# Optimization experiments

Measured on AMD Instinct MI355X. Metric: run time of the kernel, lower is better.

## Reference

```python
import jax, jax.numpy as jnp
import numpy as np

LSTM_IN = 125
LSTM_H = 125
MLP_D_H = 512
N = 512


def _lstm_scan(x, Wih, Whh, bih, bhh):
    # x: (N, LSTM_IN); PyTorch gate order: i, f, g, o
    H = LSTM_H
    def step(carry, xt):
        h, c = carry
        g = Wih @ xt + Whh @ h + bih + bhh  # (4H,)
        i = jax.nn.sigmoid(g[:H])
        f = jax.nn.sigmoid(g[H:2 * H])
        gg = jnp.tanh(g[2 * H:3 * H])
        o = jax.nn.sigmoid(g[3 * H:])
        c = f * c + i * gg
        h = o * jnp.tanh(c)
        return (h, c), h
    init = (jnp.zeros((H,), x.dtype), jnp.zeros((H,), x.dtype))
    _, hs = jax.lax.scan(step, init, x)
    return hs  # (N, H)


def setup_inputs() -> dict:
    key = jax.random.key(0)
    ks = jax.random.split(key, 14)
    s = 0.05
    d = {
        "sentence_emb": jax.random.normal(ks[0], (N, 1, LSTM_IN), jnp.float32),
        "Wih_f": jax.random.normal(ks[1], (4 * LSTM_H, LSTM_IN), jnp.float32) * s,
        "Whh_f": jax.random.normal(ks[2], (4 * LSTM_H, LSTM_H), jnp.float32) * s,
        "bih_f": jax.random.normal(ks[3], (4 * LSTM_H,), jnp.float32) * s,
        "bhh_f": jax.random.normal(ks[4], (4 * LSTM_H,), jnp.float32) * s,
        "Wih_b": jax.random.normal(ks[5], (4 * LSTM_H, LSTM_IN), jnp.float32) * s,
        "Whh_b": jax.random.normal(ks[6], (4 * LSTM_H, LSTM_H), jnp.float32) * s,
        "bih_b": jax.random.normal(ks[7], (4 * LSTM_H,), jnp.float32) * s,
        "bhh_b": jax.random.normal(ks[8], (4 * LSTM_H,), jnp.float32) * s,
        "W1": jax.random.normal(ks[9], (MLP_D_H, 4 * LSTM_H), jnp.float32) * s,
        "b1": jax.random.normal(ks[10], (MLP_D_H,), jnp.float32) * s,
        "W2": jax.random.normal(ks[11], (1, MLP_D_H), jnp.float32) * s,
        "b2": jax.random.normal(ks[12], (1,), jnp.float32) * s,
    }
    return d


def reference(sentence_emb, Wih_f, Whh_f, bih_f, bhh_f, Wih_b, Whh_b, bih_b, bhh_b, W1, b1, W2, b2):
    x = sentence_emb[:, 0, :]  # (N, 125), batch=1
    h_fwd = _lstm_scan(x, Wih_f, Whh_f, bih_f, bhh_f)           # (N, 125)
    h_bwd = _lstm_scan(x[::-1], Wih_b, Whh_b, bih_b, bhh_b)[::-1]  # (N, 125)
    h = jnp.concatenate([h_fwd, h_bwd], axis=-1)  # (N, 250)
    # output_mtx[i, j] = MLP(concat(h[j], h[i]))
    # Decompose first linear: W1 @ cat(h_j, h_i) = Wa @ h_j + Wb @ h_i
    D = h.shape[-1]
    Pa = h @ W1[:, :D].T   # (N, H): contribution of h_j
    Pb = h @ W1[:, D:].T   # (N, H): contribution of h_i
    hidden = jnp.tanh(Pb[:, None, :] + Pa[None, :, :] + b1)  # (N, N, H)
    out = hidden @ W2[0] + b2[0]  # (N, N)
    return out
```

## Files before the change

### kernel.cpp

```cpp
#include <hip/hip_runtime.h>

typedef __bf16 bf16_t;
typedef __bf16 bf16x8 __attribute__((ext_vector_type(8)));
typedef float f32x4 __attribute__((ext_vector_type(4)));
typedef int   int4v __attribute__((ext_vector_type(4)));

#define LOG2E 1.4426950408889634f

template<int CTRL>
__device__ __forceinline__ float qperm(float x) {
  return __builtin_bit_cast(float,
      __builtin_amdgcn_update_dpp(0, __builtin_bit_cast(int, x), CTRL, 0xF, 0xF, true));
}

__device__ __forceinline__ void lds_barrier() {
  asm volatile("s_waitcnt lgkmcnt(0)\n\ts_barrier" ::: "memory");
}

__global__ __launch_bounds__(256) void pre_kernel(
    const float* __restrict__ x,
    const float* __restrict__ Wih_f, const float* __restrict__ bih_f,
    const float* __restrict__ bhh_f,
    const float* __restrict__ Wih_b, const float* __restrict__ bih_b,
    const float* __restrict__ bhh_b,
    float* __restrict__ preT)
{
  const int dir = blockIdx.x >> 5;
  const int T   = blockIdx.x & 31;
  const float* __restrict__ Wih = dir ? Wih_b : Wih_f;
  const float* __restrict__ bih = dir ? bih_b : bih_f;
  const float* __restrict__ bhh = dir ? bhh_b : bhh_f;

  const int tid = threadIdx.x;
  const int wv  = tid >> 6;
  const int lane = tid & 63;
  const int q = lane >> 4, cc = lane & 15;

  const int r  = 16 * T + cc;
  const int na = r >> 2, pa = r & 3;
  const bool vld = (na < 125);
  const float* __restrict__ Wr = Wih + (vld ? (125 * pa + na) * 125 : 0);

  bf16x8 whi[4], wlo[4];
  #pragma unroll
  for (int ks = 0; ks < 4; ++ks) {
    #pragma unroll
    for (int j = 0; j < 8; ++j) {
      int k = 32 * ks + 8 * q + j;
      float wvv = (vld && k < 125) ? Wr[k] : 0.0f;
      bf16_t hi = (bf16_t)wvv;
      whi[ks][j] = hi;
      wlo[ks][j] = (bf16_t)(wvv - (float)hi);
    }
  }

  float bias[4];
  #pragma unroll
  for (int reg = 0; reg < 4; ++reg) {
    int ro = 16 * T + 4 * q + reg;
    int no = ro >> 2, po = ro & 3;
    bias[reg] = (no < 125) ? (bih[125 * po + no] + bhh[125 * po + no]) : 0.0f;
  }

  for (int i = 0; i < 8; ++i) {
    const int tt = 8 * wv + i;
    const int t  = 16 * tt + cc;
    const int trow = dir ? (511 - t) : t;
    const float* __restrict__ xr = x + trow * 125;

    f32x4 acc = (f32x4)0.0f;
    #pragma unroll
    for (int ks = 0; ks < 4; ++ks) {
      bf16x8 xhi, xlo;
      #pragma unroll
      for (int j = 0; j < 8; ++j) {
        int k = 32 * ks + 8 * q + j;
        float xv = (k < 125) ? xr[k] : 0.0f;
        bf16_t hi = (bf16_t)xv;
        xhi[j] = hi;
        xlo[j] = (bf16_t)(xv - (float)hi);
      }
      acc = __builtin_amdgcn_mfma_f32_16x16x32_bf16(whi[ks], xhi, acc, 0, 0, 0);
      acc = __builtin_amdgcn_mfma_f32_16x16x32_bf16(whi[ks], xlo, acc, 0, 0, 0);
      acc = __builtin_amdgcn_mfma_f32_16x16x32_bf16(wlo[ks], xhi, acc, 0, 0, 0);
    }
    #pragma unroll
    for (int reg = 0; reg < 4; ++reg) {
      int ro = 16 * T + 4 * q + reg;
      preT[dir * 262144 + ro * 512 + 16 * tt + cc] = acc[reg] + bias[reg];
    }
  }
}

__global__ __launch_bounds__(512) void lstm_kernel(
    const float* __restrict__ Whh_f, const float* __restrict__ Whh_b,
    const float* __restrict__ pre,
    bf16_t* __restrict__ h_all)
{
  const int dir = blockIdx.x;
  const float* __restrict__ Whh = dir ? Whh_b : Whh_f;

  const int tid  = threadIdx.x;
  const int lane = tid & 63;
  const int w    = tid >> 6;
  const int q    = lane >> 4;
  const int cc   = lane & 15;
  const int lt   = cc >> 2;
  const int p    = cc & 3;

  float wm = 0.0f;
  #pragma unroll
  for (int LT = 0; LT < 4; ++LT) {
    int rr = 16 * (4 * w + LT) + cc;
    int nn = rr >> 2, pp = rr & 3;
    if (nn < 125) {
      const float* __restrict__ Wrow = Whh + (125 * pp + nn) * 125;
      #pragma unroll
      for (int ks = 0; ks < 2; ++ks)
        #pragma unroll
        for (int jj = 0; jj < 16; ++jj) {
          int k = 64 * ks + 16 * q + jj;
          if (k < 125) wm = fmaxf(wm, fabsf(Wrow[k]));
        }
    }
  }
  #pragma unroll
  for (int off = 1; off < 64; off <<= 1)
    wm = fmaxf(wm, __shfl_xor(wm, off));
  __shared__ float wmx[8];
  if (lane == 0) wmx[w] = wm;
  __syncthreads();
  float wmax = wmx[0];
  #pragma unroll
  for (int u = 1; u < 8; ++u) wmax = fmaxf(wmax, wmx[u]);
  const float s_w  = 127.0f / wmax;
  const float invq = wmax / (127.0f * 127.0f);

  int4v afrag[4][2];
  #pragma unroll
  for (int LT = 0; LT < 4; ++LT) {
    int rr = 16 * (4 * w + LT) + cc;
    int nn = rr >> 2, pp = rr & 3;
    bool avld = (nn < 125);
    const float* __restrict__ Wrow = Whh + (avld ? (125 * pp + nn) * 125 : 0);
    #pragma unroll
    for (int ks = 0; ks < 2; ++ks) {
      int4v v;
      #pragma unroll
      for (int word = 0; word < 4; ++word) {
        int b = 0;
        #pragma unroll
        for (int byte = 0; byte < 4; ++byte) {
          int jj = 4 * word + byte;
          int k  = 64 * ks + 16 * q + jj;
          int qv = 0;
          if (avld && k < 125)
            qv = (int)__builtin_rintf(Wrow[k] * s_w);
          b |= (qv & 0xFF) << (8 * byte);
        }
        v[word] = b;
      }
      afrag[LT][ks] = v;
    }
  }

  __shared__ __align__(16) char hbuf[2][128];
  if (tid < 256) hbuf[tid >> 7][tid & 127] = 0;
  if (dir == 0) {
    #pragma unroll
    for (int u = 0; u < 6; ++u) h_all[tid * 256 + 250 + u] = (bf16_t)0.0f;
  }
  __syncthreads();

  const int   r_lane = 64 * w + 16 * lt + 4 * q + p;
  const int   nset   = 16 * w + 4 * lt + q;
  const float mult   = (p == 2) ? (-2.0f * LOG2E) : (-LOG2E);
  const float sA     = (p == 2) ? 2.0f : 1.0f;
  const float sB     = (p == 2) ? -1.0f : 0.0f;
  const float dscale = mult * invq;
  const float* __restrict__ preR = pre + dir * 262144 + r_lane * 512;
  float c = 0.0f;

  float4 pv_cur = *(const float4*)preR;

  for (int g = 0; g < 128; ++g) {
    float4 pv_nxt = make_float4(0.f, 0.f, 0.f, 0.f);
    if (g < 127) pv_nxt = *(const float4*)(preR + 4 * (g + 1));

    #pragma unroll
    for (int s4 = 0; s4 < 4; ++s4) {
      const int step = 4 * g + s4;
      const int cur  = s4 & 1, nxt = cur ^ 1;
      const float pv = (s4 == 0) ? pv_cur.x : (s4 == 1) ? pv_cur.y
                     : (s4 == 2) ? pv_cur.z : pv_cur.w;
      const float pvm = mult * pv;

      int4v b0 = *(const int4v*)&hbuf[cur][16 * q];
      int4v b1 = *(const int4v*)&hbuf[cur][64 + 16 * q];

      int4v acc[4];
      #pragma unroll
      for (int LT = 0; LT < 4; ++LT) {
        int4v a = (int4v)0;
        a = __builtin_amdgcn_mfma_i32_16x16x64_i8(afrag[LT][0], b0, a, 0, 0, 0);
        a = __builtin_amdgcn_mfma_i32_16x16x64_i8(afrag[LT][1], b1, a, 0, 0, 0);
        acc[LT] = a;
      }

      int gl[4];
      #pragma unroll
      for (int LT = 0; LT < 4; ++LT) {
        int a01 = (p & 1) ? acc[LT][1] : acc[LT][0];
        int a23 = (p & 1) ? acc[LT][3] : acc[LT][2];
        gl[LT] = (p & 2) ? a23 : a01;
      }
      int b01 = (lt & 1) ? gl[1] : gl[0];
      int b23 = (lt & 1) ? gl[3] : gl[2];
      int gsel = (lt & 2) ? b23 : b01;

      float gf  = (float)gsel;
      float xg  = fmaf(gf, dscale, pvm);
      float e   = __builtin_amdgcn_exp2f(xg);
      float y   = __builtin_amdgcn_rcpf(1.0f + e);
      float act = fmaf(y, sA, sB);

      float b_i = qperm<0x00>(act);
      float b_f = qperm<0x55>(act);
      float b_g = qperm<0xAA>(act);
      float b_o = qperm<0xFF>(act);
      c = fmaf(b_f, c, b_i * b_g);
      float e2 = __builtin_amdgcn_exp2f(-2.0f * LOG2E * c);
      float tc = fmaf(__builtin_amdgcn_rcpf(1.0f + e2), 2.0f, -1.0f);
      float h  = b_o * tc;

      if (p == 0) {
        int qh = (int)__builtin_rintf(h * 127.0f);
        hbuf[nxt][nset] = (char)qh;
        if (nset < 125) {
          int t_orig = dir ? (511 - step) : step;
          h_all[t_orig * 256 + dir * 125 + nset] = (bf16_t)h;
        }
      }
      lds_barrier();
    }
    pv_cur = pv_nxt;
  }
}

__global__ __launch_bounds__(256) void qgemm_kernel(
    const bf16_t* __restrict__ h_all,
    const float* __restrict__ W1,
    const float* __restrict__ b1,
    float* __restrict__ Ea,
    float* __restrict__ Eb)
{
  const int tid  = threadIdx.x;
  const int wv   = tid >> 6;
  const int lane = tid & 63;
  const int q    = lane >> 4, cc = lane & 15;
  const int bj   = blockIdx.x & 31;
  const int bm   = blockIdx.x >> 5;
  const int m    = bm * 64 + wv * 16 + cc;
  const int j0   = bj * 16;
  const int jA   = j0 + cc;

  const bool isB = (m >= 512);
  const int  row = isB ? (m - 512) : m;
  const int  cof = isB ? 250 : 0;

  f32x4 acc = (f32x4)0.0f;
  #pragma unroll
  for (int ks = 0; ks < 8; ++ks) {
    int kb = 32 * ks + 8 * q;
    bf16x8 a = *(const bf16x8*)&h_all[jA * 256 + kb];
    bf16x8 b;
    #pragma unroll
    for (int jj = 0; jj < 8; ++jj) {
      int k = kb + jj;
      float v = (k < 250) ? W1[row * 500 + cof + k] : 0.0f;
      b[jj] = (bf16_t)v;
    }
    acc = __builtin_amdgcn_mfma_f32_16x16x32_bf16(a, b, acc, 0, 0, 0);
  }

  const float C2 = 2.0f * LOG2E;
  #pragma unroll
  for (int reg = 0; reg < 4; ++reg) {
    int j = j0 + 4 * q + reg;
    float v = acc[reg];
    if (!isB) Ea[j * 512 + m] = __builtin_amdgcn_exp2f(C2 * v);
    else      Eb[j * 512 + (m - 512)] =
                  __builtin_amdgcn_exp2f(C2 * (v + b1[m - 512]));
  }
}

__global__ __launch_bounds__(256) void outer_kernel(
    const float* __restrict__ Ea, const float* __restrict__ Eb,
    const float* __restrict__ W2, const float* __restrict__ b2,
    float* __restrict__ out)
{
  __shared__ float sa[2][32][33];
  __shared__ float sb[2][32][33];
  __shared__ float sw[2][32];

  const int tid = threadIdx.x;
  const int bi  = blockIdx.x >> 4, bjx = blockIdx.x & 15;
  const int i0  = bi * 32, j0 = bjx * 32;
  const int ii0 = (tid & 15) * 2;
  const int jj0 = (tid >> 4) * 2;
  const int ljj = tid & 31, kk4 = (tid >> 5) * 4;

  float accR[2][2] = {{0.0f, 0.0f}, {0.0f, 0.0f}};
  float wsum = 0.0f;

  for (int kc = 0; kc < 16; ++kc) {
    const int buf = kc & 1;
    const int k0  = kc * 32;
    float4 va = *(const float4*)&Ea[(j0 + ljj) * 512 + k0 + kk4];
    float4 vb = *(const float4*)&Eb[(i0 + ljj) * 512 + k0 + kk4];
    sa[buf][kk4 + 0][ljj] = va.x; sa[buf][kk4 + 1][ljj] = va.y;
    sa[buf][kk4 + 2][ljj] = va.z; sa[buf][kk4 + 3][ljj] = va.w;
    sb[buf][kk4 + 0][ljj] = vb.x; sb[buf][kk4 + 1][ljj] = vb.y;
    sb[buf][kk4 + 2][ljj] = vb.z; sb[buf][kk4 + 3][ljj] = vb.w;
    if (tid < 32) sw[buf][tid] = W2[k0 + tid];
    __syncthreads();

    #pragma unroll 4
    for (int kk = 0; kk < 32; ++kk) {
      float2 av = *(const float2*)&sa[buf][kk][jj0];
      float2 bv = *(const float2*)&sb[buf][kk][ii0];
      float wk = sw[buf][kk];
      wsum += wk;
      {
        float e = av.x * bv.x;
        accR[0][0] = fmaf(wk, __builtin_amdgcn_rcpf(1.0f + e), accR[0][0]);
      }
      {
        float e = av.y * bv.x;
        accR[0][1] = fmaf(wk, __builtin_amdgcn_rcpf(1.0f + e), accR[0][1]);
      }
      {
        float e = av.x * bv.y;
        accR[1][0] = fmaf(wk, __builtin_amdgcn_rcpf(1.0f + e), accR[1][0]);
      }
      {
        float e = av.y * bv.y;
        accR[1][1] = fmaf(wk, __builtin_amdgcn_rcpf(1.0f + e), accR[1][1]);
      }
    }
  }

  const float bb = b2[0];
  #pragma unroll
  for (int i2 = 0; i2 < 2; ++i2)
    #pragma unroll
    for (int j2 = 0; j2 < 2; ++j2)
      out[(i0 + ii0 + i2) * 512 + (j0 + jj0 + j2)] =
          wsum - 2.0f * accR[i2][j2] + bb;
}

extern "C" void kernel_launch(void* const* d_in, const int* in_sizes, int n_in,
                              void* d_out, int out_size, void* d_ws, size_t ws_size,
                              hipStream_t stream) {
  const float* emb   = (const float*)d_in[0];
  const float* Wih_f = (const float*)d_in[1];
  const float* Whh_f = (const float*)d_in[2];
  const float* bih_f = (const float*)d_in[3];
  const float* bhh_f = (const float*)d_in[4];
  const float* Wih_b = (const float*)d_in[5];
  const float* Whh_b = (const float*)d_in[6];
  const float* bih_b = (const float*)d_in[7];
  const float* bhh_b = (const float*)d_in[8];
  const float* W1    = (const float*)d_in[9];
  const float* b1    = (const float*)d_in[10];
  const float* W2    = (const float*)d_in[11];
  const float* b2    = (const float*)d_in[12];
  float* out = (float*)d_out;

  char* ws = (char*)d_ws;
  float*  pre   = (float*)ws;
  bf16_t* h_all = (bf16_t*)(ws + 2 * 1024 * 1024);
  float*  Ea    = (float*)(ws + 2 * 1024 * 1024 + 256 * 1024);
  float*  Eb    = Ea + 512 * 512;

  pre_kernel<<<64, 256, 0, stream>>>(emb, Wih_f, bih_f, bhh_f,
                                     Wih_b, bih_b, bhh_b, pre);
  lstm_kernel<<<2, 512, 0, stream>>>(Whh_f, Whh_b, pre, h_all);
  qgemm_kernel<<<512, 256, 0, stream>>>(h_all, W1, b1, Ea, Eb);
  outer_kernel<<<256, 256, 0, stream>>>(Ea, Eb, W2, b2, out);
}
```

Baseline: 324.8 us.

## Pair k-terms in outer kernel to halve reciprocals and retile to 16x32 blocks

The outer tanh-MLP kernel now folds two consecutive k terms into one fraction, (w1*t2 + w2*t1)/(t1*t2), so each pair of hidden units needs one rcp instead of two. Tiles shrink to 16x32 outputs per block, with each thread computing two outputs, and the grid doubles to 512 blocks. Shared memory is switched to row-major k-contiguous storage so global loads can be written with float4 stores. The trade-off is a risk of overflow in the product of two exponentials when values are large, and smaller tiles that reuse each loaded value less.

```diff
diff --git a/kernel.cpp b/kernel.cpp
--- a/kernel.cpp
+++ b/kernel.cpp
@@ -299,64 +299,64 @@
     const float* __restrict__ W2, const float* __restrict__ b2,
     float* __restrict__ out)
 {
-  __shared__ float sa[2][32][33];
-  __shared__ float sb[2][32][33];
+  __shared__ float sa2[2][32][36];
+  __shared__ float sb2[2][16][36];
   __shared__ float sw[2][32];
 
   const int tid = threadIdx.x;
-  const int bi  = blockIdx.x >> 4, bjx = blockIdx.x & 15;
-  const int i0  = bi * 32, j0 = bjx * 32;
-  const int ii0 = (tid & 15) * 2;
-  const int jj0 = (tid >> 4) * 2;
-  const int ljj = tid & 31, kk4 = (tid >> 5) * 4;
-
-  float accR[2][2] = {{0.0f, 0.0f}, {0.0f, 0.0f}};
+  const int bi  = blockIdx.x >> 4;
+  const int bjx = blockIdx.x & 15;
+  const int i0  = bi * 16, j0 = bjx * 32;
+  const int ii  = tid & 15;
+  const int jj2 = tid >> 4;
+
+  const int lj  = tid & 31, lk4 = (tid >> 5) * 4;
+  const int li  = tid & 15, lk4b = ((tid >> 4) & 7) * 4;
+
+  float accR0 = 0.0f, accR1 = 0.0f;
   float wsum = 0.0f;
 
   for (int kc = 0; kc < 16; ++kc) {
     const int buf = kc & 1;
     const int k0  = kc * 32;
-    float4 va = *(const float4*)&Ea[(j0 + ljj) * 512 + k0 + kk4];
-    float4 vb = *(const float4*)&Eb[(i0 + ljj) * 512 + k0 + kk4];
-    sa[buf][kk4 + 0][ljj] = va.x; sa[buf][kk4 + 1][ljj] = va.y;
-    sa[buf][kk4 + 2][ljj] = va.z; sa[buf][kk4 + 3][ljj] = va.w;
-    sb[buf][kk4 + 0][ljj] = vb.x; sb[buf][kk4 + 1][ljj] = vb.y;
-    sb[buf][kk4 + 2][ljj] = vb.z; sb[buf][kk4 + 3][ljj] = vb.w;
+    float4 va = *(const float4*)&Ea[(j0 + lj) * 512 + k0 + lk4];
+    *(float4*)&sa2[buf][lj][lk4] = va;
+    if (tid < 128) {
+      float4 vb = *(const float4*)&Eb[(i0 + li) * 512 + k0 + lk4b];
+      *(float4*)&sb2[buf][li][lk4b] = vb;
+    }
     if (tid < 32) sw[buf][tid] = W2[k0 + tid];
     __syncthreads();
 
     #pragma unroll 4
-    for (int kk = 0; kk < 32; ++kk) {
-      float2 av = *(const float2*)&sa[buf][kk][jj0];
-      float2 bv = *(const float2*)&sb[buf][kk][ii0];
-      float wk = sw[buf][kk];
-      wsum += wk;
+    for (int kk = 0; kk < 32; kk += 2) {
+      float2 wv = *(const float2*)&sw[buf][kk];
+      float2 bv = *(const float2*)&sb2[buf][ii][kk];
+      float2 a0 = *(const float2*)&sa2[buf][2 * jj2 + 0][kk];
+      float2 a1 = *(const float2*)&sa2[buf][2 * jj2 + 1][kk];
+      wsum += wv.x + wv.y;
       {
-        float e = av.x * bv.x;
-        accR[0][0] = fmaf(wk, __builtin_amdgcn_rcpf(1.0f + e), accR[0][0]);
+        float t1  = fmaf(a0.x, bv.x, 1.0f);
+        float t2  = fmaf(a0.y, bv.y, 1.0f);
+        float den = t1 * t2;
+        float num = fmaf(wv.x, t2, wv.y * t1);
+        accR0 = fmaf(num, __builtin_amdgcn_rcpf(den), accR0);
       }
       {
-        float e = av.y * bv.x;
-        accR[0][1] = fmaf(wk, __builtin_amdgcn_rcpf(1.0f + e), accR[0][1]);
-      }
-      {
-        float e = av.x * bv.y;
-        accR[1][0] = fmaf(wk, __builtin_amdgcn_rcpf(1.0f + e), accR[1][0]);
-      }
-      {
-        float e = av.y * bv.y;
-        accR[1][1] = fmaf(wk, __builtin_amdgcn_rcpf(1.0f + e), accR[1][1]);
+        float t1  = fmaf(a1.x, bv.x, 1.0f);
+        float t2  = fmaf(a1.y, bv.y, 1.0f);
+        float den = t1 * t2;
+        float num = fmaf(wv.x, t2, wv.y * t1);
+        accR1 = fmaf(num, __builtin_amdgcn_rcpf(den), accR1);
       }
     }
   }
 
   const float bb = b2[0];
-  #pragma unroll
-  for (int i2 = 0; i2 < 2; ++i2)
-    #pragma unroll
-    for (int j2 = 0; j2 < 2; ++j2)
-      out[(i0 + ii0 + i2) * 512 + (j0 + jj0 + j2)] =
-          wsum - 2.0f * accR[i2][j2] + bb;
+  float2 o;
+  o.x = wsum - 2.0f * accR0 + bb;
+  o.y = wsum - 2.0f * accR1 + bb;
+  *(float2*)&out[(i0 + ii) * 512 + j0 + 2 * jj2] = o;
 }
 
 extern "C" void kernel_launch(void* const* d_in, const int* in_sizes, int n_in,
@@ -387,5 +387,5 @@
                                      Wih_b, bih_b, bhh_b, pre);
   lstm_kernel<<<2, 512, 0, stream>>>(Whh_f, Whh_b, pre, h_all);
   qgemm_kernel<<<512, 256, 0, stream>>>(h_all, W1, b1, Ea, Eb);
-  outer_kernel<<<256, 256, 0, stream>>>(Ea, Eb, W2, b2, out);
-}
+  outer_kernel<<<512, 256, 0, stream>>>(Ea, Eb, W2, b2, out);
+}
```

After: 318.9 us. No clear change (-1.8%).
